# Optimization experiments

Measured on AMD Instinct MI355X. Metric: run time of the kernel, lower is better.

Reference implementation:

```python
import jax, jax.numpy as jnp
import numpy as np

N, E, D, H, L = 100000, 1600000, 128, 64, 3
BN_EPS = 1e-5


def setup_inputs() -> dict:
    key = jax.random.key(0)
    ks = iter(jax.random.split(key, 32))
    r = lambda shape, s=0.05: jax.random.normal(next(ks), shape, dtype=jnp.float32) * s
    inp = {
        "x": jax.random.normal(next(ks), (N, D), dtype=jnp.float32),
        "edge_index": jax.random.randint(next(ks), (2, E), 0, N, dtype=jnp.int64),
        "fa_W1": r((D, H)), "fa_b1": jnp.zeros((H,), jnp.float32),
        "fa_W2": r((H, D)), "fa_b2": jnp.zeros((D,), jnp.float32),
        "proj_W": r((D, H)), "proj_b": jnp.zeros((H,), jnp.float32),
        "gat_W": r((L, H, H)), "gat_asrc": r((L, H)), "gat_adst": r((L, H)),
        "gat_b": jnp.zeros((L, H), jnp.float32),
        "bn_gamma": jnp.ones((L, H), jnp.float32), "bn_beta": jnp.zeros((L, H), jnp.float32),
        "bn_mean": jnp.zeros((L, H), jnp.float32), "bn_var": jnp.ones((L, H), jnp.float32),
        "se_W1": r((3, H // 2)), "se_b1": jnp.zeros((H // 2,), jnp.float32),
        "se_W2": r((H // 2, H)), "se_b2": jnp.zeros((H,), jnp.float32),
        "out_W1": r((2 * H, H)), "out_b1": jnp.zeros((H,), jnp.float32),
        "out_W2": r((H, H // 2)), "out_b2": jnp.zeros((H // 2,), jnp.float32),
        "out_W3": r((H // 2, 1)), "out_b3": jnp.zeros((1,), jnp.float32),
    }
    return inp


def _gat_layer(h, src, dst, n, W, a_src, a_dst, b):
    # PyG GATConv (heads=1, self-loops already appended to src/dst).
    z = h @ W                              # [N,H]
    e = jax.nn.leaky_relu((z @ a_src)[src] + (z @ a_dst)[dst], 0.2)  # [Etot]
    m = jax.ops.segment_max(e, dst, num_segments=n)
    m = jnp.where(jnp.isfinite(m), m, 0.0)
    ex = jnp.exp(e - m[dst])
    denom = jax.ops.segment_sum(ex, dst, num_segments=n)
    alpha = ex / denom[dst]
    return jax.ops.segment_sum(z[src] * alpha[:, None], dst, num_segments=n) + b


def _structural(edge_index, n, dtype):
    src, dst = edge_index[0], edge_index[1]
    deg = jax.ops.segment_sum(jnp.ones(src.shape, dtype), src, num_segments=n)
    norm_deg = deg / jnp.maximum(deg.max(), 1.0)
    infl_sum = jax.ops.segment_sum(deg[dst], src, num_segments=n)
    infl = jnp.where(deg > 0, infl_sum / jnp.maximum(deg, 1.0), 0.0)
    infl = infl / jnp.maximum(infl.max(), 1e-12)
    return jnp.stack([norm_deg, jnp.zeros_like(deg), infl], axis=1)  # [N,3]


def reference(x, edge_index, fa_W1, fa_b1, fa_W2, fa_b2, proj_W, proj_b,
              gat_W, gat_asrc, gat_adst, gat_b, bn_gamma, bn_beta, bn_mean, bn_var,
              se_W1, se_b1, se_W2, se_b2, out_W1, out_b1, out_W2, out_b2, out_W3, out_b3):
    n = x.shape[0]
    # feature attention
    fw = jax.nn.sigmoid(jnp.maximum(x @ fa_W1 + fa_b1, 0.0) @ fa_W2 + fa_b2)
    h = (x * fw) @ proj_W + proj_b
    # self loops for GAT
    loop = jnp.arange(n, dtype=edge_index.dtype)
    src = jnp.concatenate([edge_index[0], loop])
    dst = jnp.concatenate([edge_index[1], loop])
    for l in range(L):
        h = _gat_layer(h, src, dst, n, gat_W[l], gat_asrc[l], gat_adst[l], gat_b[l])
        h = (h - bn_mean[l]) * jax.lax.rsqrt(bn_var[l] + BN_EPS) * bn_gamma[l] + bn_beta[l]
        h = jnp.maximum(h, 0.0)  # eval mode: dropout is identity
    sf = _structural(edge_index, n, h.dtype)
    se = jnp.maximum(sf @ se_W1 + se_b1, 0.0) @ se_W2 + se_b2
    h = jnp.concatenate([h, se], axis=1)  # [N, 2H]
    o = jnp.maximum(h @ out_W1 + out_b1, 0.0)
    o = jnp.maximum(o @ out_W2 + out_b2, 0.0)
    return jax.nn.sigmoid(o @ out_W3 + out_b3)
```

## Files before the change

### kernel.cpp

```cpp
#include <hip/hip_runtime.h>


typedef unsigned int uint;
typedef __attribute__((ext_vector_type(8))) short bf16x8;
typedef __attribute__((ext_vector_type(4))) float f32x4;

__device__ __forceinline__ uint f2bf(float a) {
    uint u = __float_as_uint(a);
    return (u + 0x7fffu + ((u >> 16) & 1u)) >> 16;
}
__device__ __forceinline__ float bflo(uint p) { return __uint_as_float(p << 16); }
__device__ __forceinline__ float bfhi(uint p) { return __uint_as_float(p & 0xffff0000u); }

__device__ __forceinline__ void packOne(const float* W, int C, int KS,
                                        unsigned short* dst, int o) {
    int j = o & 7, lane = (o >> 3) & 63, f = o >> 9;
    int ks = f % KS, ct = f / KS;
    int row = 32 * ks + 8 * (lane >> 4) + j;
    int col = ct * 16 + (lane & 15);
    dst[o] = (unsigned short)f2bf(W[row * C + col]);
}

__global__ void k_pack(const float* __restrict__ faW1, const float* __restrict__ faW2,
                       const float* __restrict__ projW, const float* __restrict__ gatW,
                       unsigned short* __restrict__ pA, unsigned short* __restrict__ pB,
                       unsigned short* __restrict__ pC, unsigned short* __restrict__ pG) {
    int i = blockIdx.x * blockDim.x + threadIdx.x;
    if (i < 8192) packOne(faW1, 64, 4, pA, i);
    else if (i < 16384) packOne(faW2, 128, 2, pB, i - 8192);
    else if (i < 24576) packOne(projW, 64, 4, pC, i - 16384);
    else if (i < 36864) {
        int o = i - 24576; int l = o >> 12;
        packOne(gatW + l * 4096, 64, 2, pG + l * 4096, o & 4095);
    }
}

__global__ __attribute__((amdgpu_waves_per_eu(4, 4))) void __launch_bounds__(256)
k_fused1(const float* __restrict__ x,
         const unsigned short* __restrict__ pA, const float* __restrict__ fab1,
         const unsigned short* __restrict__ pB, const float* __restrict__ fab2,
         const unsigned short* __restrict__ pC, const float* __restrict__ projb,
         float* __restrict__ hbuf, int N,
         const int* __restrict__ ei, int E,
         float* __restrict__ deg, int* __restrict__ cursor, int* __restrict__ esrc,
         const float* __restrict__ seW2, const float* __restrict__ seb2,
         const float* __restrict__ oW1, const float* __restrict__ ob1,
         float* __restrict__ M2, float* __restrict__ b2f,
         int gMlp, int gEdge) {
    __shared__ float S[4][16][132];
    int bid = blockIdx.x;
    if (bid < gMlp) {
        int wave = threadIdx.x >> 6, lane = threadIdx.x & 63;
        int qg = lane >> 4, lr = lane & 15;
        int n0w = (bid * 4 + wave) * 16;
        int nr = n0w + lr; if (nr >= N) nr = N - 1;
        const float* xr = x + (size_t)nr * 128;
        float (*T)[132] = S[wave];
        const bf16x8* fA = reinterpret_cast<const bf16x8*>(pA);
        const bf16x8* fB = reinterpret_cast<const bf16x8*>(pB);
        const bf16x8* fC = reinterpret_cast<const bf16x8*>(pC);

        bf16x8 afr[4];
#pragma unroll
        for (int ks = 0; ks < 4; ++ks) {
            const float* p = xr + 32 * ks + 8 * qg;
            float4 v0 = *reinterpret_cast<const float4*>(p);
            float4 v1 = *reinterpret_cast<const float4*>(p + 4);
            bf16x8 a;
            a[0] = (short)f2bf(v0.x); a[1] = (short)f2bf(v0.y);
            a[2] = (short)f2bf(v0.z); a[3] = (short)f2bf(v0.w);
            a[4] = (short)f2bf(v1.x); a[5] = (short)f2bf(v1.y);
            a[6] = (short)f2bf(v1.z); a[7] = (short)f2bf(v1.w);
            afr[ks] = a;
        }
        {
            f32x4 acc[4] = {{0,0,0,0},{0,0,0,0},{0,0,0,0},{0,0,0,0}};
#pragma unroll
            for (int ct = 0; ct < 4; ++ct)
#pragma unroll
                for (int ks = 0; ks < 4; ++ks)
                    acc[ct] = __builtin_amdgcn_mfma_f32_16x16x32_bf16(
                        afr[ks], fA[(ct * 4 + ks) * 64 + lane], acc[ct], 0, 0, 0);
#pragma unroll
            for (int ct = 0; ct < 4; ++ct) {
                float b1v = fab1[ct * 16 + lr];
#pragma unroll
                for (int r = 0; r < 4; ++r)
                    T[qg * 4 + r][ct * 16 + lr] = fmaxf(acc[ct][r] + b1v, 0.f);
            }
        }
        __syncthreads();

        bf16x8 bfr[2];
#pragma unroll
        for (int ks = 0; ks < 2; ++ks) {
            const float* p = &T[lr][32 * ks + 8 * qg];
            float4 v0 = *reinterpret_cast<const float4*>(p);
            float4 v1 = *reinterpret_cast<const float4*>(p + 4);
            bf16x8 a;
            a[0] = (short)f2bf(v0.x); a[1] = (short)f2bf(v0.y);
            a[2] = (short)f2bf(v0.z); a[3] = (short)f2bf(v0.w);
            a[4] = (short)f2bf(v1.x); a[5] = (short)f2bf(v1.y);
            a[6] = (short)f2bf(v1.z); a[7] = (short)f2bf(v1.w);
            bfr[ks] = a;
        }
        __syncthreads();
        {
            f32x4 acc[8] = {{0,0,0,0},{0,0,0,0},{0,0,0,0},{0,0,0,0},
                            {0,0,0,0},{0,0,0,0},{0,0,0,0},{0,0,0,0}};
#pragma unroll
            for (int ct = 0; ct < 8; ++ct)
#pragma unroll
                for (int ks = 0; ks < 2; ++ks)
                    acc[ct] = __builtin_amdgcn_mfma_f32_16x16x32_bf16(
                        bfr[ks], fB[(ct * 2 + ks) * 64 + lane], acc[ct], 0, 0, 0);
#pragma unroll
            for (int ct = 0; ct < 8; ++ct) {
                float b2v = fab2[ct * 16 + lr];
#pragma unroll
                for (int r = 0; r < 4; ++r)
                    T[qg * 4 + r][ct * 16 + lr] = acc[ct][r] + b2v;
            }
        }
        __syncthreads();

        bf16x8 cfr[4];
#pragma unroll
        for (int ks = 0; ks < 4; ++ks) {
            const float* pf = &T[lr][32 * ks + 8 * qg];
            const float* px = xr + 32 * ks + 8 * qg;
            float4 f0 = *reinterpret_cast<const float4*>(pf);
            float4 f1 = *reinterpret_cast<const float4*>(pf + 4);
            float4 x0 = *reinterpret_cast<const float4*>(px);
            float4 x1 = *reinterpret_cast<const float4*>(px + 4);
            bf16x8 a;
            a[0] = (short)f2bf(x0.x / (1.f + __expf(-f0.x)));
            a[1] = (short)f2bf(x0.y / (1.f + __expf(-f0.y)));
            a[2] = (short)f2bf(x0.z / (1.f + __expf(-f0.z)));
            a[3] = (short)f2bf(x0.w / (1.f + __expf(-f0.w)));
            a[4] = (short)f2bf(x1.x / (1.f + __expf(-f1.x)));
            a[5] = (short)f2bf(x1.y / (1.f + __expf(-f1.y)));
            a[6] = (short)f2bf(x1.z / (1.f + __expf(-f1.z)));
            a[7] = (short)f2bf(x1.w / (1.f + __expf(-f1.w)));
            cfr[ks] = a;
        }
        __syncthreads();
        {
            f32x4 acc[4] = {{0,0,0,0},{0,0,0,0},{0,0,0,0},{0,0,0,0}};
#pragma unroll
            for (int ct = 0; ct < 4; ++ct)
#pragma unroll
                for (int ks = 0; ks < 4; ++ks)
                    acc[ct] = __builtin_amdgcn_mfma_f32_16x16x32_bf16(
                        cfr[ks], fC[(ct * 4 + ks) * 64 + lane], acc[ct], 0, 0, 0);
#pragma unroll
            for (int ct = 0; ct < 4; ++ct) {
                float pbv = projb[ct * 16 + lr];
#pragma unroll
                for (int r = 0; r < 4; ++r)
                    T[qg * 4 + r][ct * 16 + lr] = acc[ct][r] + pbv;
            }
        }
        __syncthreads();
        int n = n0w + lr;
        if (n < N) {
            float* hr = hbuf + (size_t)n * 64 + qg * 16;
            const float* sr = &T[lr][qg * 16];
#pragma unroll
            for (int q4 = 0; q4 < 4; ++q4)
                *reinterpret_cast<float4*>(hr + q4 * 4) =
                    *reinterpret_cast<const float4*>(sr + q4 * 4);
            if (qg == 0) esrc[(size_t)n * 64] = n;
        }
    } else if (bid < gMlp + gEdge) {
        int e = (bid - gMlp) * blockDim.x + threadIdx.x;
        if (e < E) {
            int s = ei[e], d = ei[E + e];
            atomicAdd(&deg[s], 1.f);
            int p = atomicAdd(&cursor[d], 1);
            esrc[(size_t)d * 64 + 1 + p] = s;
        }
    } else {
        int tid = threadIdx.x;
        for (int o = tid; o < 32 * 64; o += 256) {
            int k = o >> 6, j = o & 63;
            float s = 0.f;
            for (int i = 0; i < 64; ++i)
                s = fmaf(seW2[k * 64 + i], oW1[(64 + i) * 64 + j], s);
            M2[o] = s;
        }
        for (int j = tid; j < 64; j += 256) {
            float s = ob1[j];
            for (int i = 0; i < 64; ++i)
                s = fmaf(seb2[i], oW1[(64 + i) * 64 + j], s);
            b2f[j] = s;
        }
    }
}

__global__ __attribute__((amdgpu_waves_per_eu(4, 4))) void __launch_bounds__(256)
k_z(const float* __restrict__ hbuf, const unsigned short* __restrict__ pWz,
    const float* __restrict__ asrc, const float* __restrict__ adst,
    uint* __restrict__ zbuf, float* __restrict__ es, float* __restrict__ ed,
    const int* __restrict__ ei, int E,
    const float* __restrict__ deg, float* __restrict__ inflsum,
    float* __restrict__ inflv, unsigned* __restrict__ scal,
    int N, int gZ, int riderMode) {
    int bid = blockIdx.x;
    if (bid >= gZ) {
        if (riderMode == 1) {
            int e = (bid - gZ) * blockDim.x + threadIdx.x;
            if (e < E) atomicAdd(&inflsum[ei[e]], deg[ei[E + e]]);
        } else {
            int idx = (bid - gZ) * blockDim.x + threadIdx.x;
            float dv = 0.f, iv = 0.f;
            if (idx < N) {
                dv = deg[idx];
                iv = dv > 0.f ? inflsum[idx] / dv : 0.f;
                inflv[idx] = iv;
            }
            float dm = dv, im = iv;
#pragma unroll
            for (int off = 32; off; off >>= 1) {
                dm = fmaxf(dm, __shfl_xor(dm, off, 64));
                im = fmaxf(im, __shfl_xor(im, off, 64));
            }
            if ((threadIdx.x & 63) == 0) {
                atomicMax(scal + 0, __float_as_uint(dm));
                atomicMax(scal + 1, __float_as_uint(im));
            }
        }
        return;
    }
    __shared__ float zt[4][16][68];
    int wave = threadIdx.x >> 6, lane = threadIdx.x & 63;
    int qg = lane >> 4, lr = lane & 15;
    int n0w = (bid * 4 + wave) * 16;
    int nr = n0w + lr; if (nr >= N) nr = N - 1;

    bf16x8 afr[2];
#pragma unroll
    for (int k2 = 0; k2 < 2; ++k2) {
        const float* hp = hbuf + (size_t)nr * 64 + k2 * 32 + qg * 8;
        float4 h0 = *reinterpret_cast<const float4*>(hp);
        float4 h1 = *reinterpret_cast<const float4*>(hp + 4);
        bf16x8 a;
        a[0] = (short)f2bf(h0.x); a[1] = (short)f2bf(h0.y);
        a[2] = (short)f2bf(h0.z); a[3] = (short)f2bf(h0.w);
        a[4] = (short)f2bf(h1.x); a[5] = (short)f2bf(h1.y);
        a[6] = (short)f2bf(h1.z); a[7] = (short)f2bf(h1.w);
        afr[k2] = a;
    }

    const bf16x8* pw = reinterpret_cast<const bf16x8*>(pWz);
    f32x4 acc0 = {0,0,0,0}, acc1 = {0,0,0,0}, acc2 = {0,0,0,0}, acc3 = {0,0,0,0};
#pragma unroll
    for (int k2 = 0; k2 < 2; ++k2) {
        acc0 = __builtin_amdgcn_mfma_f32_16x16x32_bf16(afr[k2], pw[(0 * 2 + k2) * 64 + lane], acc0, 0, 0, 0);
        acc1 = __builtin_amdgcn_mfma_f32_16x16x32_bf16(afr[k2], pw[(1 * 2 + k2) * 64 + lane], acc1, 0, 0, 0);
        acc2 = __builtin_amdgcn_mfma_f32_16x16x32_bf16(afr[k2], pw[(2 * 2 + k2) * 64 + lane], acc2, 0, 0, 0);
        acc3 = __builtin_amdgcn_mfma_f32_16x16x32_bf16(afr[k2], pw[(3 * 2 + k2) * 64 + lane], acc3, 0, 0, 0);
    }

    float (*Z)[68] = zt[wave];
#pragma unroll
    for (int r = 0; r < 4; ++r) {
        Z[qg * 4 + r][0 * 16 + lr] = acc0[r];
        Z[qg * 4 + r][1 * 16 + lr] = acc1[r];
        Z[qg * 4 + r][2 * 16 + lr] = acc2[r];
        Z[qg * 4 + r][3 * 16 + lr] = acc3[r];
    }
    __syncthreads();

    float zr[16];
    const float* zrow = &Z[lr][qg * 16];
#pragma unroll
    for (int q4 = 0; q4 < 4; ++q4) {
        float4 v = *reinterpret_cast<const float4*>(zrow + q4 * 4);
        zr[q4 * 4] = v.x; zr[q4 * 4 + 1] = v.y; zr[q4 * 4 + 2] = v.z; zr[q4 * 4 + 3] = v.w;
    }
    float pe = 0.f, pd = 0.f;
#pragma unroll
    for (int j = 0; j < 16; ++j) {
        pe = fmaf(zr[j], asrc[qg * 16 + j], pe);
        pd = fmaf(zr[j], adst[qg * 16 + j], pd);
    }
    pe += __shfl_xor(pe, 16, 64); pe += __shfl_xor(pe, 32, 64);
    pd += __shfl_xor(pd, 16, 64); pd += __shfl_xor(pd, 32, 64);

    int n = n0w + lr;
    if (n < N) {
        uint4 u0, u1;
        u0.x = f2bf(zr[0]) | (f2bf(zr[1]) << 16);
        u0.y = f2bf(zr[2]) | (f2bf(zr[3]) << 16);
        u0.z = f2bf(zr[4]) | (f2bf(zr[5]) << 16);
        u0.w = f2bf(zr[6]) | (f2bf(zr[7]) << 16);
        u1.x = f2bf(zr[8]) | (f2bf(zr[9]) << 16);
        u1.y = f2bf(zr[10]) | (f2bf(zr[11]) << 16);
        u1.z = f2bf(zr[12]) | (f2bf(zr[13]) << 16);
        u1.w = f2bf(zr[14]) | (f2bf(zr[15]) << 16);
        uint* zr8 = zbuf + (size_t)n * 32 + qg * 8;
        *reinterpret_cast<uint4*>(zr8) = u0;
        *reinterpret_cast<uint4*>(zr8 + 4) = u1;
        if (qg == 0) { es[n] = pe; ed[n] = pd; }
    }
}

__global__ void k_agg(const int* __restrict__ cursor,
                      const int* __restrict__ esrc,
                      const float* __restrict__ es, const float* __restrict__ ed,
                      const uint* __restrict__ zb,
                      const float* __restrict__ b, const float* __restrict__ g,
                      const float* __restrict__ bta, const float* __restrict__ mean,
                      const float* __restrict__ var,
                      float* __restrict__ hbuf, int N) {
    int wid  = (blockIdx.x * blockDim.x + threadIdx.x) >> 6;
    int lane = threadIdx.x & 63;
    if (wid >= N) return;
    size_t row0 = (size_t)wid * 64;
    int c    = cursor[wid] + 1;
    float edn = ed[wid];
    int lq = lane & 15, q = lane >> 4;

    int   sreg = 0;
    float exv  = 0.f;
    if (lane < c) {
        sreg = esrc[row0 + lane];
        float e = es[sreg] + edn;
        e = e >= 0.f ? e : 0.2f * e;
        exv = __expf(e);
    }
    float ssum = exv;
#pragma unroll
    for (int off = 32; off; off >>= 1) ssum += __shfl_xor(ssum, off, 64);

    float a0 = 0.f, a1 = 0.f, a2 = 0.f, a3 = 0.f;
    for (int e = q; e < c; e += 4) {
        int   se = __shfl(sreg, e, 64);
        float we = __shfl(exv, e, 64);
        uint2 p = *reinterpret_cast<const uint2*>(zb + (size_t)se * 32 + lq * 2);
        a0 = fmaf(bflo(p.x), we, a0);
        a1 = fmaf(bfhi(p.x), we, a1);
        a2 = fmaf(bflo(p.y), we, a2);
        a3 = fmaf(bfhi(p.y), we, a3);
    }
    a0 += __shfl_xor(a0, 16, 64); a0 += __shfl_xor(a0, 32, 64);
    a1 += __shfl_xor(a1, 16, 64); a1 += __shfl_xor(a1, 32, 64);
    a2 += __shfl_xor(a2, 16, 64); a2 += __shfl_xor(a2, 32, 64);
    a3 += __shfl_xor(a3, 16, 64); a3 += __shfl_xor(a3, 32, 64);

    if (q == 0) {
        float inv = 1.f / ssum;
        float4 bb = reinterpret_cast<const float4*>(b)[lq];
        float4 gg = reinterpret_cast<const float4*>(g)[lq];
        float4 tt = reinterpret_cast<const float4*>(bta)[lq];
        float4 mm = reinterpret_cast<const float4*>(mean)[lq];
        float4 vv = reinterpret_cast<const float4*>(var)[lq];
        float v0 = (a0 * inv + bb.x - mm.x) * (gg.x * rsqrtf(vv.x + 1e-5f)) + tt.x;
        float v1 = (a1 * inv + bb.y - mm.y) * (gg.y * rsqrtf(vv.y + 1e-5f)) + tt.y;
        float v2 = (a2 * inv + bb.z - mm.z) * (gg.z * rsqrtf(vv.z + 1e-5f)) + tt.z;
        float v3 = (a3 * inv + bb.w - mm.w) * (gg.w * rsqrtf(vv.w + 1e-5f)) + tt.w;
        reinterpret_cast<float4*>(hbuf + (size_t)wid * 64)[lq] =
            make_float4(fmaxf(v0, 0.f), fmaxf(v1, 0.f), fmaxf(v2, 0.f), fmaxf(v3, 0.f));
    }
}

__global__ __attribute__((amdgpu_waves_per_eu(4, 4))) void __launch_bounds__(256)
k_final(const float* __restrict__ hbuf, const float* __restrict__ deg,
        const float* __restrict__ inflv, const unsigned* __restrict__ scal,
        const float* __restrict__ seW1, const float* __restrict__ seb1,
        const float* __restrict__ M2, const float* __restrict__ b2f,
        const float* __restrict__ oW1,
        const float* __restrict__ oW2, const float* __restrict__ ob2,
        const float* __restrict__ oW3, const float* __restrict__ ob3,
        float* __restrict__ out, int N) {
    int tid = blockIdx.x * blockDim.x + threadIdx.x;
    int n = tid < N ? tid : N - 1;

    float degmax  = fmaxf(__uint_as_float(scal[0]), 1.0f);
    float inflmax = fmaxf(__uint_as_float(scal[1]), 1e-12f);
    float nd = deg[n] / degmax;
    float fl = inflv[n] / inflmax;

    float hid[32];
#pragma unroll
    for (int k = 0; k < 32; ++k)
        hid[k] = fmaxf(fmaf(nd, seW1[k], fmaf(fl, seW1[64 + k], seb1[k])), 0.f);

    float o1[64];
#pragma unroll
    for (int j = 0; j < 64; ++j) o1[j] = b2f[j];
#pragma unroll 4
    for (int k = 0; k < 32; ++k) {
#pragma unroll
        for (int j = 0; j < 64; ++j)
            o1[j] = fmaf(hid[k], M2[k * 64 + j], o1[j]);
    }
    const float* hr = hbuf + (size_t)n * 64;
#pragma unroll 2
    for (int c = 0; c < 16; ++c) {
        float4 hv = *reinterpret_cast<const float4*>(hr + c * 4);
        const float* wb = oW1 + c * 4 * 64;
#pragma unroll
        for (int j = 0; j < 64; ++j) {
            o1[j] = fmaf(hv.x, wb[j], o1[j]);
            o1[j] = fmaf(hv.y, wb[64 + j], o1[j]);
            o1[j] = fmaf(hv.z, wb[128 + j], o1[j]);
            o1[j] = fmaf(hv.w, wb[192 + j], o1[j]);
        }
    }
#pragma unroll
    for (int j = 0; j < 64; ++j) o1[j] = fmaxf(o1[j], 0.f);

    float o2[32];
#pragma unroll
    for (int k = 0; k < 32; ++k) o2[k] = ob2[k];
#pragma unroll 4
    for (int j = 0; j < 64; ++j) {
#pragma unroll
        for (int k = 0; k < 32; ++k)
            o2[k] = fmaf(o1[j], oW2[j * 32 + k], o2[k]);
    }
    float a0 = 0, a1 = 0, a2 = 0, a3 = 0;
#pragma unroll
    for (int k = 0; k < 32; k += 4) {
        a0 = fmaf(fmaxf(o2[k], 0.f), oW3[k], a0);
        a1 = fmaf(fmaxf(o2[k + 1], 0.f), oW3[k + 1], a1);
        a2 = fmaf(fmaxf(o2[k + 2], 0.f), oW3[k + 2], a2);
        a3 = fmaf(fmaxf(o2[k + 3], 0.f), oW3[k + 3], a3);
    }
    if (tid < N)
        out[tid] = 1.f / (1.f + __expf(-((a0 + a1) + (a2 + a3) + ob3[0])));
}

extern "C" void kernel_launch(void* const* d_in, const int* in_sizes, int n_in,
                              void* d_out, int out_size, void* d_ws, size_t ws_size,
                              hipStream_t stream) {
    const float* x     = (const float*)d_in[0];
    const int*   ei    = (const int*)d_in[1];
    const float* faW1  = (const float*)d_in[2];
    const float* fab1  = (const float*)d_in[3];
    const float* faW2  = (const float*)d_in[4];
    const float* fab2  = (const float*)d_in[5];
    const float* projW = (const float*)d_in[6];
    const float* projb = (const float*)d_in[7];
    const float* gatW  = (const float*)d_in[8];
    const float* gatAs = (const float*)d_in[9];
    const float* gatAd = (const float*)d_in[10];
    const float* gatB  = (const float*)d_in[11];
    const float* bnG   = (const float*)d_in[12];
    const float* bnB   = (const float*)d_in[13];
    const float* bnM   = (const float*)d_in[14];
    const float* bnV   = (const float*)d_in[15];
    const float* seW1  = (const float*)d_in[16];
    const float* seb1  = (const float*)d_in[17];
    const float* seW2  = (const float*)d_in[18];
    const float* seb2  = (const float*)d_in[19];
    const float* oW1   = (const float*)d_in[20];
    const float* ob1   = (const float*)d_in[21];
    const float* oW2   = (const float*)d_in[22];
    const float* ob2   = (const float*)d_in[23];
    const float* oW3   = (const float*)d_in[24];
    const float* ob3   = (const float*)d_in[25];
    float* out = (float*)d_out;

    const int N = in_sizes[0] / 128;
    const int E = in_sizes[1] / 2;

    float* ws      = (float*)d_ws;
    float* hbuf    = ws;
    uint*  zbuf    = (uint*)(hbuf + (size_t)N * 64);
    float* es      = (float*)(zbuf + (size_t)N * 32);
    float* ed      = es + N;
    float* deg     = ed + N;
    float* inflsum = deg + N;
    unsigned* scal = (unsigned*)(inflsum + N);
    int* cursor    = (int*)(scal + 8);
    float* inflv   = (float*)(cursor + N);
    int* esrc      = (int*)(inflv + N);
    float* M2      = (float*)(esrc + (size_t)N * 64);
    float* b2f     = M2 + 32 * 64;
    unsigned short* pA  = (unsigned short*)(b2f + 64);
    unsigned short* pB  = pA + 8192;
    unsigned short* pC  = pB + 8192;
    unsigned short* pWz = pC + 8192;

    dim3 blk(256);
    int gN    = (N + 255) / 256;
    int gE    = (E + 255) / 256;
    int gM    = (N + 63) / 64;
    int gZm   = (N + 63) / 64;
    int blkNW = (N * 64 + 255) / 256;

    hipMemsetAsync(deg, 0, ((size_t)3 * N + 8) * sizeof(float), stream);

    k_pack<<<144, blk, 0, stream>>>(faW1, faW2, projW, gatW, pA, pB, pC, pWz);

    k_fused1<<<gM + gE + 1, blk, 0, stream>>>(x, pA, fab1, pB, fab2, pC, projb,
                                              hbuf, N, ei, E, deg, cursor, esrc,
                                              seW2, seb2, oW1, ob1, M2, b2f, gM, gE);

    for (int l = 0; l < 3; ++l) {
        int extra = (l == 0) ? gE : (l == 1 ? gN : 0);
        int mode  = (l == 0) ? 1  : (l == 1 ? 2  : 0);
        k_z<<<gZm + extra, blk, 0, stream>>>(hbuf, pWz + l * 4096, gatAs + l * 64,
                                             gatAd + l * 64, zbuf, es, ed,
                                             ei, E, deg, inflsum, inflv, scal,
                                             N, gZm, mode);
        k_agg<<<blkNW, blk, 0, stream>>>(cursor, esrc, es, ed, zbuf,
                                         gatB + l * 64, bnG + l * 64, bnB + l * 64,
                                         bnM + l * 64, bnV + l * 64, hbuf, N);
    }

    k_final<<<gN, blk, 0, stream>>>(hbuf, deg, inflv, scal, seW1, seb1, M2, b2f,
                                    oW1, oW2, ob2, oW3, ob3, out, N);
}
```

Measured before the change: 620.7 us.

## Move output MLP to bf16 MFMA and store LDS intermediates as bf16

The final per-node scalar MLP, which ran 64x64 and 64x32 FMAs in registers per thread, is rewritten as wave-level bf16 MFMA tiles over 16 nodes. It uses newly packed oW1, oW2 and M2 fragments, and the last dot product becomes a lane shuffle reduction. In the fused feature-attention kernel, intermediates in LDS are stored as bf16 instead of fp32, one barrier is removed, and hbuf is written directly from the accumulators. The waves_per_eu hints are dropped from two kernels. The aim is to cut scalar FMA and register pressure in the final kernel and LDS traffic in the first, at the cost of bf16 rounding on the output MLP.

```diff
diff --git a/kernel.cpp b/kernel.cpp
--- a/kernel.cpp
+++ b/kernel.cpp
@@ -2,6 +2,7 @@
 
 
 typedef unsigned int uint;
+typedef unsigned short ushort;
 typedef __attribute__((ext_vector_type(8))) short bf16x8;
 typedef __attribute__((ext_vector_type(4))) float f32x4;
 
@@ -11,20 +12,23 @@
 }
 __device__ __forceinline__ float bflo(uint p) { return __uint_as_float(p << 16); }
 __device__ __forceinline__ float bfhi(uint p) { return __uint_as_float(p & 0xffff0000u); }
+__device__ __forceinline__ float b2f16(ushort u) { return __uint_as_float((uint)u << 16); }
 
 __device__ __forceinline__ void packOne(const float* W, int C, int KS,
-                                        unsigned short* dst, int o) {
+                                        ushort* dst, int o) {
     int j = o & 7, lane = (o >> 3) & 63, f = o >> 9;
     int ks = f % KS, ct = f / KS;
     int row = 32 * ks + 8 * (lane >> 4) + j;
     int col = ct * 16 + (lane & 15);
-    dst[o] = (unsigned short)f2bf(W[row * C + col]);
+    dst[o] = (ushort)f2bf(W[row * C + col]);
 }
 
 __global__ void k_pack(const float* __restrict__ faW1, const float* __restrict__ faW2,
                        const float* __restrict__ projW, const float* __restrict__ gatW,
-                       unsigned short* __restrict__ pA, unsigned short* __restrict__ pB,
-                       unsigned short* __restrict__ pC, unsigned short* __restrict__ pG) {
+                       const float* __restrict__ oW1, const float* __restrict__ oW2,
+                       ushort* __restrict__ pA, ushort* __restrict__ pB,
+                       ushort* __restrict__ pC, ushort* __restrict__ pG,
+                       ushort* __restrict__ pO1u, ushort* __restrict__ pOW2) {
     int i = blockIdx.x * blockDim.x + threadIdx.x;
     if (i < 8192) packOne(faW1, 64, 4, pA, i);
     else if (i < 16384) packOne(faW2, 128, 2, pB, i - 8192);
@@ -32,22 +36,23 @@
     else if (i < 36864) {
         int o = i - 24576; int l = o >> 12;
         packOne(gatW + l * 4096, 64, 2, pG + l * 4096, o & 4095);
-    }
-}
-
-__global__ __attribute__((amdgpu_waves_per_eu(4, 4))) void __launch_bounds__(256)
+    } else if (i < 40960) packOne(oW1, 64, 2, pO1u, i - 36864);
+    else if (i < 43008) packOne(oW2, 32, 2, pOW2, i - 40960);
+}
+
+__global__ void __launch_bounds__(256)
 k_fused1(const float* __restrict__ x,
-         const unsigned short* __restrict__ pA, const float* __restrict__ fab1,
-         const unsigned short* __restrict__ pB, const float* __restrict__ fab2,
-         const unsigned short* __restrict__ pC, const float* __restrict__ projb,
+         const ushort* __restrict__ pA, const float* __restrict__ fab1,
+         const ushort* __restrict__ pB, const float* __restrict__ fab2,
+         const ushort* __restrict__ pC, const float* __restrict__ projb,
          float* __restrict__ hbuf, int N,
          const int* __restrict__ ei, int E,
          float* __restrict__ deg, int* __restrict__ cursor, int* __restrict__ esrc,
          const float* __restrict__ seW2, const float* __restrict__ seb2,
          const float* __restrict__ oW1, const float* __restrict__ ob1,
-         float* __restrict__ M2, float* __restrict__ b2f,
+         float* __restrict__ M2, float* __restrict__ b2f, ushort* __restrict__ pM2f,
          int gMlp, int gEdge) {
-    __shared__ float S[4][16][132];
+    __shared__ ushort S[4][16][136];
     int bid = blockIdx.x;
     if (bid < gMlp) {
         int wave = threadIdx.x >> 6, lane = threadIdx.x & 63;
@@ -55,7 +60,7 @@
         int n0w = (bid * 4 + wave) * 16;
         int nr = n0w + lr; if (nr >= N) nr = N - 1;
         const float* xr = x + (size_t)nr * 128;
-        float (*T)[132] = S[wave];
+        ushort (*T)[136] = S[wave];
         const bf16x8* fA = reinterpret_cast<const bf16x8*>(pA);
         const bf16x8* fB = reinterpret_cast<const bf16x8*>(pB);
         const bf16x8* fC = reinterpret_cast<const bf16x8*>(pC);
@@ -86,24 +91,16 @@
                 float b1v = fab1[ct * 16 + lr];
 #pragma unroll
                 for (int r = 0; r < 4; ++r)
-                    T[qg * 4 + r][ct * 16 + lr] = fmaxf(acc[ct][r] + b1v, 0.f);
+                    T[qg * 4 + r][ct * 16 + lr] =
+                        (ushort)f2bf(fmaxf(acc[ct][r] + b1v, 0.f));
             }
         }
         __syncthreads();
 
         bf16x8 bfr[2];
 #pragma unroll
-        for (int ks = 0; ks < 2; ++ks) {
-            const float* p = &T[lr][32 * ks + 8 * qg];
-            float4 v0 = *reinterpret_cast<const float4*>(p);
-            float4 v1 = *reinterpret_cast<const float4*>(p + 4);
-            bf16x8 a;
-            a[0] = (short)f2bf(v0.x); a[1] = (short)f2bf(v0.y);
-            a[2] = (short)f2bf(v0.z); a[3] = (short)f2bf(v0.w);
-            a[4] = (short)f2bf(v1.x); a[5] = (short)f2bf(v1.y);
-            a[6] = (short)f2bf(v1.z); a[7] = (short)f2bf(v1.w);
-            bfr[ks] = a;
-        }
+        for (int ks = 0; ks < 2; ++ks)
+            bfr[ks] = *reinterpret_cast<const bf16x8*>(&T[lr][32 * ks + 8 * qg]);
         __syncthreads();
         {
             f32x4 acc[8] = {{0,0,0,0},{0,0,0,0},{0,0,0,0},{0,0,0,0},
@@ -119,7 +116,7 @@
                 float b2v = fab2[ct * 16 + lr];
 #pragma unroll
                 for (int r = 0; r < 4; ++r)
-                    T[qg * 4 + r][ct * 16 + lr] = acc[ct][r] + b2v;
+                    T[qg * 4 + r][ct * 16 + lr] = (ushort)f2bf(acc[ct][r] + b2v);
             }
         }
         __syncthreads();
@@ -127,24 +124,21 @@
         bf16x8 cfr[4];
 #pragma unroll
         for (int ks = 0; ks < 4; ++ks) {
-            const float* pf = &T[lr][32 * ks + 8 * qg];
+            const ushort* pf = &T[lr][32 * ks + 8 * qg];
             const float* px = xr + 32 * ks + 8 * qg;
-            float4 f0 = *reinterpret_cast<const float4*>(pf);
-            float4 f1 = *reinterpret_cast<const float4*>(pf + 4);
             float4 x0 = *reinterpret_cast<const float4*>(px);
             float4 x1 = *reinterpret_cast<const float4*>(px + 4);
             bf16x8 a;
-            a[0] = (short)f2bf(x0.x / (1.f + __expf(-f0.x)));
-            a[1] = (short)f2bf(x0.y / (1.f + __expf(-f0.y)));
-            a[2] = (short)f2bf(x0.z / (1.f + __expf(-f0.z)));
-            a[3] = (short)f2bf(x0.w / (1.f + __expf(-f0.w)));
-            a[4] = (short)f2bf(x1.x / (1.f + __expf(-f1.x)));
-            a[5] = (short)f2bf(x1.y / (1.f + __expf(-f1.y)));
-            a[6] = (short)f2bf(x1.z / (1.f + __expf(-f1.z)));
-            a[7] = (short)f2bf(x1.w / (1.f + __expf(-f1.w)));
+            a[0] = (short)f2bf(x0.x / (1.f + __expf(-b2f16(pf[0]))));
+            a[1] = (short)f2bf(x0.y / (1.f + __expf(-b2f16(pf[1]))));
+            a[2] = (short)f2bf(x0.z / (1.f + __expf(-b2f16(pf[2]))));
+            a[3] = (short)f2bf(x0.w / (1.f + __expf(-b2f16(pf[3]))));
+            a[4] = (short)f2bf(x1.x / (1.f + __expf(-b2f16(pf[4]))));
+            a[5] = (short)f2bf(x1.y / (1.f + __expf(-b2f16(pf[5]))));
+            a[6] = (short)f2bf(x1.z / (1.f + __expf(-b2f16(pf[6]))));
+            a[7] = (short)f2bf(x1.w / (1.f + __expf(-b2f16(pf[7]))));
             cfr[ks] = a;
         }
-        __syncthreads();
         {
             f32x4 acc[4] = {{0,0,0,0},{0,0,0,0},{0,0,0,0},{0,0,0,0}};
 #pragma unroll
@@ -154,23 +148,16 @@
                     acc[ct] = __builtin_amdgcn_mfma_f32_16x16x32_bf16(
                         cfr[ks], fC[(ct * 4 + ks) * 64 + lane], acc[ct], 0, 0, 0);
 #pragma unroll
-            for (int ct = 0; ct < 4; ++ct) {
-                float pbv = projb[ct * 16 + lr];
-#pragma unroll
-                for (int r = 0; r < 4; ++r)
-                    T[qg * 4 + r][ct * 16 + lr] = acc[ct][r] + pbv;
+            for (int r = 0; r < 4; ++r) {
+                int n = n0w + qg * 4 + r;
+                if (n < N) {
+#pragma unroll
+                    for (int ct = 0; ct < 4; ++ct)
+                        hbuf[(size_t)n * 64 + ct * 16 + lr] =
+                            acc[ct][r] + projb[ct * 16 + lr];
+                    if (lr == 0) esrc[(size_t)n * 64] = n;
+                }
             }
-        }
-        __syncthreads();
-        int n = n0w + lr;
-        if (n < N) {
-            float* hr = hbuf + (size_t)n * 64 + qg * 16;
-            const float* sr = &T[lr][qg * 16];
-#pragma unroll
-            for (int q4 = 0; q4 < 4; ++q4)
-                *reinterpret_cast<float4*>(hr + q4 * 4) =
-                    *reinterpret_cast<const float4*>(sr + q4 * 4);
-            if (qg == 0) esrc[(size_t)n * 64] = n;
         }
     } else if (bid < gMlp + gEdge) {
         int e = (bid - gMlp) * blockDim.x + threadIdx.x;
@@ -195,11 +182,14 @@
                 s = fmaf(seb2[i], oW1[(64 + i) * 64 + j], s);
             b2f[j] = s;
         }
+        __syncthreads();
+        for (int o = tid; o < 2048; o += 256)
+            packOne(M2, 64, 1, pM2f, o);
     }
 }
 
 __global__ __attribute__((amdgpu_waves_per_eu(4, 4))) void __launch_bounds__(256)
-k_z(const float* __restrict__ hbuf, const unsigned short* __restrict__ pWz,
+k_z(const float* __restrict__ hbuf, const ushort* __restrict__ pWz,
     const float* __restrict__ asrc, const float* __restrict__ adst,
     uint* __restrict__ zbuf, float* __restrict__ es, float* __restrict__ ed,
     const int* __restrict__ ei, int E,
@@ -365,72 +355,97 @@
     }
 }
 
-__global__ __attribute__((amdgpu_waves_per_eu(4, 4))) void __launch_bounds__(256)
+__global__ void __launch_bounds__(256)
 k_final(const float* __restrict__ hbuf, const float* __restrict__ deg,
         const float* __restrict__ inflv, const unsigned* __restrict__ scal,
         const float* __restrict__ seW1, const float* __restrict__ seb1,
-        const float* __restrict__ M2, const float* __restrict__ b2f,
-        const float* __restrict__ oW1,
-        const float* __restrict__ oW2, const float* __restrict__ ob2,
+        const ushort* __restrict__ pM2f, const float* __restrict__ b2f,
+        const ushort* __restrict__ pO1u, const ushort* __restrict__ pOW2,
+        const float* __restrict__ ob2,
         const float* __restrict__ oW3, const float* __restrict__ ob3,
         float* __restrict__ out, int N) {
-    int tid = blockIdx.x * blockDim.x + threadIdx.x;
-    int n = tid < N ? tid : N - 1;
+    __shared__ ushort S[4][16][136];
+    int wave = threadIdx.x >> 6, lane = threadIdx.x & 63;
+    int qg = lane >> 4, lr = lane & 15;
+    int n0w = (blockIdx.x * 4 + wave) * 16;
+    int nr = n0w + lr; if (nr >= N) nr = N - 1;
+    ushort (*T)[136] = S[wave];
 
     float degmax  = fmaxf(__uint_as_float(scal[0]), 1.0f);
     float inflmax = fmaxf(__uint_as_float(scal[1]), 1e-12f);
-    float nd = deg[n] / degmax;
-    float fl = inflv[n] / inflmax;
-
-    float hid[32];
-#pragma unroll
-    for (int k = 0; k < 32; ++k)
-        hid[k] = fmaxf(fmaf(nd, seW1[k], fmaf(fl, seW1[64 + k], seb1[k])), 0.f);
-
-    float o1[64];
-#pragma unroll
-    for (int j = 0; j < 64; ++j) o1[j] = b2f[j];
-#pragma unroll 4
-    for (int k = 0; k < 32; ++k) {
-#pragma unroll
-        for (int j = 0; j < 64; ++j)
-            o1[j] = fmaf(hid[k], M2[k * 64 + j], o1[j]);
-    }
-    const float* hr = hbuf + (size_t)n * 64;
-#pragma unroll 2
-    for (int c = 0; c < 16; ++c) {
-        float4 hv = *reinterpret_cast<const float4*>(hr + c * 4);
-        const float* wb = oW1 + c * 4 * 64;
-#pragma unroll
-        for (int j = 0; j < 64; ++j) {
-            o1[j] = fmaf(hv.x, wb[j], o1[j]);
-            o1[j] = fmaf(hv.y, wb[64 + j], o1[j]);
-            o1[j] = fmaf(hv.z, wb[128 + j], o1[j]);
-            o1[j] = fmaf(hv.w, wb[192 + j], o1[j]);
-        }
-    }
-#pragma unroll
-    for (int j = 0; j < 64; ++j) o1[j] = fmaxf(o1[j], 0.f);
-
-    float o2[32];
-#pragma unroll
-    for (int k = 0; k < 32; ++k) o2[k] = ob2[k];
-#pragma unroll 4
-    for (int j = 0; j < 64; ++j) {
-#pragma unroll
-        for (int k = 0; k < 32; ++k)
-            o2[k] = fmaf(o1[j], oW2[j * 32 + k], o2[k]);
-    }
-    float a0 = 0, a1 = 0, a2 = 0, a3 = 0;
-#pragma unroll
-    for (int k = 0; k < 32; k += 4) {
-        a0 = fmaf(fmaxf(o2[k], 0.f), oW3[k], a0);
-        a1 = fmaf(fmaxf(o2[k + 1], 0.f), oW3[k + 1], a1);
-        a2 = fmaf(fmaxf(o2[k + 2], 0.f), oW3[k + 2], a2);
-        a3 = fmaf(fmaxf(o2[k + 3], 0.f), oW3[k + 3], a3);
-    }
-    if (tid < N)
-        out[tid] = 1.f / (1.f + __expf(-((a0 + a1) + (a2 + a3) + ob3[0])));
+    float nd = deg[nr] / degmax;
+    float fl = inflv[nr] / inflmax;
+
+    bf16x8 a0, a1, a2;
+#pragma unroll
+    for (int ks = 0; ks < 2; ++ks) {
+        const float* hp = hbuf + (size_t)nr * 64 + 32 * ks + 8 * qg;
+        float4 h0 = *reinterpret_cast<const float4*>(hp);
+        float4 h1 = *reinterpret_cast<const float4*>(hp + 4);
+        bf16x8 a;
+        a[0] = (short)f2bf(h0.x); a[1] = (short)f2bf(h0.y);
+        a[2] = (short)f2bf(h0.z); a[3] = (short)f2bf(h0.w);
+        a[4] = (short)f2bf(h1.x); a[5] = (short)f2bf(h1.y);
+        a[6] = (short)f2bf(h1.z); a[7] = (short)f2bf(h1.w);
+        if (ks == 0) a0 = a; else a1 = a;
+    }
+#pragma unroll
+    for (int j = 0; j < 8; ++j) {
+        int k = 8 * qg + j;
+        float hid = fmaxf(fmaf(nd, seW1[k], fmaf(fl, seW1[64 + k], seb1[k])), 0.f);
+        a2[j] = (short)f2bf(hid);
+    }
+
+    const bf16x8* fO1 = reinterpret_cast<const bf16x8*>(pO1u);
+    const bf16x8* fM2 = reinterpret_cast<const bf16x8*>(pM2f);
+    const bf16x8* fW2 = reinterpret_cast<const bf16x8*>(pOW2);
+
+    {
+        f32x4 acc[4] = {{0,0,0,0},{0,0,0,0},{0,0,0,0},{0,0,0,0}};
+#pragma unroll
+        for (int ct = 0; ct < 4; ++ct) {
+            acc[ct] = __builtin_amdgcn_mfma_f32_16x16x32_bf16(a0, fO1[(ct * 2 + 0) * 64 + lane], acc[ct], 0, 0, 0);
+            acc[ct] = __builtin_amdgcn_mfma_f32_16x16x32_bf16(a1, fO1[(ct * 2 + 1) * 64 + lane], acc[ct], 0, 0, 0);
+            acc[ct] = __builtin_amdgcn_mfma_f32_16x16x32_bf16(a2, fM2[ct * 64 + lane], acc[ct], 0, 0, 0);
+        }
+#pragma unroll
+        for (int ct = 0; ct < 4; ++ct) {
+            float bv = b2f[ct * 16 + lr];
+#pragma unroll
+            for (int r = 0; r < 4; ++r)
+                T[qg * 4 + r][ct * 16 + lr] =
+                    (ushort)f2bf(fmaxf(acc[ct][r] + bv, 0.f));
+        }
+    }
+    __syncthreads();
+
+    bf16x8 b0 = *reinterpret_cast<const bf16x8*>(&T[lr][8 * qg]);
+    bf16x8 b1 = *reinterpret_cast<const bf16x8*>(&T[lr][32 + 8 * qg]);
+    f32x4 o2a = {0,0,0,0}, o2b = {0,0,0,0};
+    o2a = __builtin_amdgcn_mfma_f32_16x16x32_bf16(b0, fW2[0 * 64 + lane], o2a, 0, 0, 0);
+    o2a = __builtin_amdgcn_mfma_f32_16x16x32_bf16(b1, fW2[1 * 64 + lane], o2a, 0, 0, 0);
+    o2b = __builtin_amdgcn_mfma_f32_16x16x32_bf16(b0, fW2[2 * 64 + lane], o2b, 0, 0, 0);
+    o2b = __builtin_amdgcn_mfma_f32_16x16x32_bf16(b1, fW2[3 * 64 + lane], o2b, 0, 0, 0);
+
+    float w3a = oW3[lr], w3b = oW3[16 + lr];
+    float oba = ob2[lr], obb = ob2[16 + lr];
+    float part[4];
+#pragma unroll
+    for (int r = 0; r < 4; ++r)
+        part[r] = fmaxf(o2a[r] + oba, 0.f) * w3a + fmaxf(o2b[r] + obb, 0.f) * w3b;
+#pragma unroll
+    for (int off = 1; off < 16; off <<= 1) {
+#pragma unroll
+        for (int r = 0; r < 4; ++r) part[r] += __shfl_xor(part[r], off, 64);
+    }
+    if (lr == 0) {
+        float b3 = ob3[0];
+#pragma unroll
+        for (int r = 0; r < 4; ++r) {
+            int n = n0w + qg * 4 + r;
+            if (n < N) out[n] = 1.f / (1.f + __expf(-(part[r] + b3)));
+        }
+    }
 }
 
 extern "C" void kernel_launch(void* const* d_in, const int* in_sizes, int n_in,
@@ -480,38 +495,42 @@
     int* esrc      = (int*)(inflv + N);
     float* M2      = (float*)(esrc + (size_t)N * 64);
     float* b2f     = M2 + 32 * 64;
-    unsigned short* pA  = (unsigned short*)(b2f + 64);
-    unsigned short* pB  = pA + 8192;
-    unsigned short* pC  = pB + 8192;
-    unsigned short* pWz = pC + 8192;
+    ushort* pA   = (ushort*)(b2f + 64);
+    ushort* pB   = pA + 8192;
+    ushort* pC   = pB + 8192;
+    ushort* pWz  = pC + 8192;
+    ushort* pO1u = pWz + 3 * 4096;
+    ushort* pOW2 = pO1u + 4096;
+    ushort* pM2f = pOW2 + 2048;
 
     dim3 blk(256);
     int gN    = (N + 255) / 256;
     int gE    = (E + 255) / 256;
     int gM    = (N + 63) / 64;
-    int gZm   = (N + 63) / 64;
     int blkNW = (N * 64 + 255) / 256;
 
     hipMemsetAsync(deg, 0, ((size_t)3 * N + 8) * sizeof(float), stream);
 
-    k_pack<<<144, blk, 0, stream>>>(faW1, faW2, projW, gatW, pA, pB, pC, pWz);
+    k_pack<<<168, blk, 0, stream>>>(faW1, faW2, projW, gatW, oW1, oW2,
+                                    pA, pB, pC, pWz, pO1u, pOW2);
 
     k_fused1<<<gM + gE + 1, blk, 0, stream>>>(x, pA, fab1, pB, fab2, pC, projb,
                                               hbuf, N, ei, E, deg, cursor, esrc,
-                                              seW2, seb2, oW1, ob1, M2, b2f, gM, gE);
+                                              seW2, seb2, oW1, ob1, M2, b2f, pM2f,
+                                              gM, gE);
 
     for (int l = 0; l < 3; ++l) {
         int extra = (l == 0) ? gE : (l == 1 ? gN : 0);
         int mode  = (l == 0) ? 1  : (l == 1 ? 2  : 0);
-        k_z<<<gZm + extra, blk, 0, stream>>>(hbuf, pWz + l * 4096, gatAs + l * 64,
-                                             gatAd + l * 64, zbuf, es, ed,
-                                             ei, E, deg, inflsum, inflv, scal,
-                                             N, gZm, mode);
+        k_z<<<gM + extra, blk, 0, stream>>>(hbuf, pWz + l * 4096, gatAs + l * 64,
+                                            gatAd + l * 64, zbuf, es, ed,
+                                            ei, E, deg, inflsum, inflv, scal,
+                                            N, gM, mode);
         k_agg<<<blkNW, blk, 0, stream>>>(cursor, esrc, es, ed, zbuf,
                                          gatB + l * 64, bnG + l * 64, bnB + l * 64,
                                          bnM + l * 64, bnV + l * 64, hbuf, N);
     }
 
-    k_final<<<gN, blk, 0, stream>>>(hbuf, deg, inflv, scal, seW1, seb1, M2, b2f,
-                                    oW1, oW2, ob2, oW3, ob3, out, N);
-}
+    k_final<<<gM, blk, 0, stream>>>(hbuf, deg, inflv, scal, seW1, seb1,
+                                    pM2f, b2f, pO1u, pOW2, ob2, oW3, ob3, out, N);
+}
```

Result: faster. 517.1 us (-16.7%).
